# Kernel tuning notes

Hardware: AMD Instinct MI355X
Metric: run time of the kernel (lower is better)

The kernel has to match this reference:

```python
import jax, jax.numpy as jnp
import numpy as np

N = 50000      # nodes
E = 800000     # edges (before self-loops)
F_IN = 128     # num_node_features
H = 4          # heads
C = 32         # graph_hidden_channels (per head)
HC = H * C     # 128
NHID = 512
NOUT = 768
G = 256        # graphs in batch
NEG_SLOPE = 0.2


def setup_inputs() -> dict:
    key = jax.random.key(0)
    ks = jax.random.split(key, 32)
    s = 0.05
    inp = {
        "x": jax.random.normal(ks[0], (N, F_IN), jnp.float32),
        "edge_index": jax.random.randint(ks[1], (2, E), 0, N, jnp.int64),
        "batch": jnp.sort(jax.random.randint(ks[2], (N,), 0, G, jnp.int64)),
    }
    dims = [F_IN, HC, HC]
    k = 3
    for i, din in enumerate(dims, start=1):
        inp[f"w{i}"] = jax.random.normal(ks[k], (din, HC), jnp.float32) * s; k += 1
        inp[f"as{i}"] = jax.random.normal(ks[k], (H, C), jnp.float32) * s; k += 1
        inp[f"ad{i}"] = jax.random.normal(ks[k], (H, C), jnp.float32) * s; k += 1
        inp[f"b{i}"] = jnp.zeros((HC,), jnp.float32)
        inp[f"sk{i}w"] = jax.random.normal(ks[k], (din, HC), jnp.float32) * s; k += 1
        inp[f"sk{i}b"] = jnp.zeros((HC,), jnp.float32)
    inp["m1w"] = jax.random.normal(ks[k], (HC, NHID), jnp.float32) * s; k += 1
    inp["m1b"] = jnp.zeros((NHID,), jnp.float32)
    inp["m2w"] = jax.random.normal(ks[k], (NHID, NOUT), jnp.float32) * s
    inp["m2b"] = jnp.zeros((NOUT,), jnp.float32)
    return inp


def _gat_conv(x, src, dst, W, a_src, a_dst, b):
    # x: [N, din]; src/dst: [E+N] (self-loops included)
    n = x.shape[0]
    h = (x @ W).reshape(n, H, C)                       # [N, H, C]
    e_src = jnp.sum(h * a_src, axis=-1)                # [N, H]
    e_dst = jnp.sum(h * a_dst, axis=-1)                # [N, H]
    e = jax.nn.leaky_relu(e_src[src] + e_dst[dst], NEG_SLOPE)  # [E', H]
    m = jax.ops.segment_max(e, dst, num_segments=n)    # segment softmax (stable)
    ex = jnp.exp(e - m[dst])
    z = jax.ops.segment_sum(ex, dst, num_segments=n)
    alpha = ex / z[dst]                                # [E', H]
    out = jax.ops.segment_sum(alpha[:, :, None] * h[src], dst, num_segments=n)
    return out.reshape(n, HC) + b


def reference(x, edge_index, batch,
              w1, as1, ad1, b1, sk1w, sk1b,
              w2, as2, ad2, b2, sk2w, sk2b,
              w3, as3, ad3, b3, sk3w, sk3b,
              m1w, m1b, m2w, m2b):
    n = x.shape[0]
    loops = jnp.arange(n, dtype=edge_index.dtype)
    src = jnp.concatenate([edge_index[0], loops])      # PyG add_self_loops=True
    dst = jnp.concatenate([edge_index[1], loops])

    h = jax.nn.relu(x @ sk1w + sk1b + _gat_conv(x, src, dst, w1, as1, ad1, b1))
    h = jax.nn.relu(h @ sk2w + sk2b + _gat_conv(h, src, dst, w2, as2, ad2, b2))
    h = jax.nn.relu(h @ sk3w + sk3b + _gat_conv(h, src, dst, w3, as3, ad3, b3))

    pooled = jax.ops.segment_max(h, batch, num_segments=G)  # global_max_pool
    pooled = jnp.where(jnp.isfinite(pooled), pooled, 0.0)   # guard empty graphs
    out = jax.nn.relu(pooled @ m1w + m1b)
    out = out @ m2w + m2b
    return out
```

## Files before the change

### kernel.cpp

```cpp
#include <hip/hip_runtime.h>
#include <hip/hip_bf16.h>
#include <math.h>

#define NN 50000
#define EE 800000
#define EPE 850000
#define HCC 128
#define GGR 256
#define NHIDD 512
#define NOUTD 768
#define CHUNK 256
#define CPAD (CHUNK + 8)
#define SCAN_NBLK ((NN + 1023) / 1024)
#define MBLK ((NN + 63) / 64)
#define NPAD 50176
#define NREP 8

typedef __attribute__((ext_vector_type(8))) short bf16x8;
typedef __attribute__((ext_vector_type(4))) float f32x4;

__device__ __forceinline__ void atomicMaxF(float* addr, float v) {
    if (v >= 0.f) atomicMax(reinterpret_cast<int*>(addr), __float_as_int(v));
    else atomicMin(reinterpret_cast<unsigned int*>(addr), __float_as_uint(v));
}

__device__ __forceinline__ float lrelu(float x) { return x > 0.f ? x : 0.2f * x; }

__device__ __forceinline__ ushort f2bf(float f) {
    unsigned u = __float_as_uint(f);
    unsigned r = (u + 0x7fffu + ((u >> 16) & 1u)) >> 16;
    return (ushort)r;
}
__device__ __forceinline__ float bf2f(ushort b) {
    return __uint_as_float(((unsigned)b) << 16);
}

__global__ void conv_x(const float* __restrict__ X, ushort* __restrict__ Xb) {
    int i = blockIdx.x * 256 + threadIdx.x;
    if (i < NN * HCC / 4) {
        float4 v = reinterpret_cast<const float4*>(X)[i];
        ushort4 o;
        o.x = f2bf(v.x); o.y = f2bf(v.y); o.z = f2bf(v.z); o.w = f2bf(v.w);
        reinterpret_cast<ushort4*>(Xb)[i] = o;
    }
}

__global__ void conv_w(const float* __restrict__ W, const float* __restrict__ SKW,
                       ushort* __restrict__ Wt) {
    int i = blockIdx.x * 256 + threadIdx.x;
    if (i >= 256 * 128) return;
    int n = i >> 7, k = i & 127;
    float v = (n < 128) ? W[(size_t)k * 128 + n] : SKW[(size_t)k * 128 + (n - 128)];
    Wt[i] = f2bf(v);
}

__global__ void hist_zero8(int* __restrict__ cnt8) {
    int i = blockIdx.x * 256 + threadIdx.x;
    if (i < NREP * NPAD) cnt8[i] = 0;
}

__global__ void hist8(const int* __restrict__ ei, int* __restrict__ cnt8) {
    int e = blockIdx.x * 256 + threadIdx.x;
    if (e >= EPE) return;
    int rep = blockIdx.x & 7;
    int d = (e < EE) ? ei[EE + e] : e - EE;
    atomicAdd(&cnt8[rep * NPAD + d], 1);
}

__global__ __launch_bounds__(256) void scan_partial(const int* __restrict__ cnt8,
                                                    int* __restrict__ excl,
                                                    int* __restrict__ blocksums)
{
    __shared__ int s[256];
    const int b = blockIdx.x, t = threadIdx.x;
    const int idx = b * 1024 + t * 4;
    int a[4] = {0, 0, 0, 0};
    #pragma unroll
    for (int j = 0; j < 4; ++j) {
        if (idx + j < NN) {
            int tot = 0;
            #pragma unroll
            for (int r = 0; r < NREP; ++r) tot += cnt8[r * NPAD + idx + j];
            a[j] = tot;
        }
    }
    int sum4 = a[0] + a[1] + a[2] + a[3];
    s[t] = sum4;
    __syncthreads();
    #pragma unroll
    for (int off = 1; off < 256; off <<= 1) {
        int add = (t >= off) ? s[t - off] : 0;
        __syncthreads();
        s[t] += add;
        __syncthreads();
    }
    int e0 = s[t] - sum4;
    if (idx + 0 < NN) excl[idx + 0] = e0;
    if (idx + 1 < NN) excl[idx + 1] = e0 + a[0];
    if (idx + 2 < NN) excl[idx + 2] = e0 + a[0] + a[1];
    if (idx + 3 < NN) excl[idx + 3] = e0 + a[0] + a[1] + a[2];
    if (t == 255) blocksums[b] = s[255];
}

__global__ __launch_bounds__(64) void scan_sums(int* __restrict__ blocksums,
                                                int* __restrict__ blockoffs,
                                                int* __restrict__ row_start)
{
    __shared__ int s[64];
    int t = threadIdx.x;
    int v = (t < SCAN_NBLK) ? blocksums[t] : 0;
    s[t] = v;
    __syncthreads();
    #pragma unroll
    for (int off = 1; off < 64; off <<= 1) {
        int add = (t >= off) ? s[t - off] : 0;
        __syncthreads();
        s[t] += add;
        __syncthreads();
    }
    if (t < SCAN_NBLK) blockoffs[t] = s[t] - v;
    if (t == 63) row_start[NN] = s[63];
}

__global__ void scan_add(const int* __restrict__ excl, const int* __restrict__ blockoffs,
                         const int* __restrict__ cnt8,
                         int* __restrict__ row_start, int* __restrict__ cur8)
{
    int i = blockIdx.x * 256 + threadIdx.x;
    if (i >= NN) return;
    int v = excl[i] + blockoffs[i >> 10];
    row_start[i] = v;
    int c = v;
    #pragma unroll
    for (int r = 0; r < NREP; ++r) {
        cur8[r * NPAD + i] = c;
        c += cnt8[r * NPAD + i];
    }
}

__global__ void scatter_csr8(const int* __restrict__ ei, int* __restrict__ cur8,
                             int* __restrict__ csr_src) {
    int e = blockIdx.x * 256 + threadIdx.x;
    if (e >= EPE) return;
    int rep = blockIdx.x & 7;
    int s, d;
    if (e < EE) { s = ei[e]; d = ei[EE + e]; } else { s = d = e - EE; }
    int pos = atomicAdd(&cur8[rep * NPAD + d], 1);
    csr_src[pos] = s;
}

__global__ __launch_bounds__(256) void gemm_mfma(
    const ushort* __restrict__ Xb,
    const ushort* __restrict__ Wt,
    const float* __restrict__ skb, const float* __restrict__ bb,
    ushort* __restrict__ Hout, float* __restrict__ Agg)
{
    __shared__ ushort Xs[64 * 128];
    const int r0 = blockIdx.x * 64;
    const int tid = threadIdx.x;
    const int w = tid >> 6;
    const int l = tid & 63;
    const int lm = l & 15;
    const int lk = l >> 4;

    #pragma unroll
    for (int it = 0; it < 4; ++it) {
        int slot = it * 256 + tid;
        int row = slot >> 4;
        int bc = (slot & 15) << 4;
        int n = r0 + row;
        bf16x8 v = (bf16x8)(short)0;
        if (n < NN) v = *reinterpret_cast<const bf16x8*>(Xb + (size_t)n * 128 + (bc >> 1));
        *reinterpret_cast<bf16x8*>(reinterpret_cast<char*>(Xs) + row * 256 + (bc ^ ((row & 7) << 4))) = v;
    }
    __syncthreads();

    f32x4 acc[4][4];
    #pragma unroll
    for (int nb = 0; nb < 4; ++nb)
        #pragma unroll
        for (int rf = 0; rf < 4; ++rf)
            acc[nb][rf] = (f32x4){0.f, 0.f, 0.f, 0.f};

    #pragma unroll
    for (int ks = 0; ks < 4; ++ks) {
        bf16x8 a[4];
        #pragma unroll
        for (int rf = 0; rf < 4; ++rf) {
            int row = rf * 16 + lm;
            int bc = (ks * 32 + lk * 8) * 2;
            a[rf] = *reinterpret_cast<const bf16x8*>(
                reinterpret_cast<const char*>(Xs) + row * 256 + (bc ^ ((row & 7) << 4)));
        }
        #pragma unroll
        for (int nb = 0; nb < 4; ++nb) {
            int ncol = (w * 4 + nb) * 16 + lm;
            bf16x8 b = *reinterpret_cast<const bf16x8*>(Wt + (size_t)ncol * 128 + ks * 32 + lk * 8);
            #pragma unroll
            for (int rf = 0; rf < 4; ++rf)
                acc[nb][rf] = __builtin_amdgcn_mfma_f32_16x16x32_bf16(a[rf], b, acc[nb][rf], 0, 0, 0);
        }
    }

    #pragma unroll
    for (int nb = 0; nb < 4; ++nb) {
        int ncol = (w * 4 + nb) * 16 + lm;
        #pragma unroll
        for (int rf = 0; rf < 4; ++rf) {
            #pragma unroll
            for (int r = 0; r < 4; ++r) {
                int n = r0 + rf * 16 + lk * 4 + r;
                if (n >= NN) continue;
                float v = acc[nb][rf][r];
                if (ncol < 128) {
                    Hout[(size_t)n * 128 + ncol] = f2bf(v);
                } else {
                    int c = ncol - 128;
                    Agg[(size_t)n * 128 + c] = v + skb[c] + bb[c];
                }
            }
        }
    }
}

__global__ __launch_bounds__(256) void node_attn(
    const ushort* __restrict__ Hb, const float* __restrict__ as_, const float* __restrict__ ad_,
    float* __restrict__ esrc, float* __restrict__ edst)
{
    int tid = threadIdx.x;
    int node = blockIdx.x * 2 + (tid >> 7);
    int t = tid & 127;
    if (node >= NN) return;
    float hv = bf2f(Hb[(size_t)node * 128 + t]);
    float p1 = hv * as_[t];
    float p2 = hv * ad_[t];
    #pragma unroll
    for (int o = 16; o > 0; o >>= 1) {
        p1 += __shfl_down(p1, o, 32);
        p2 += __shfl_down(p2, o, 32);
    }
    if ((t & 31) == 0) {
        esrc[node * 4 + (t >> 5)] = p1;
        edst[node * 4 + (t >> 5)] = p2;
    }
}

__global__ __launch_bounds__(128) void gat_aggr(
    const int* __restrict__ row_start, const int* __restrict__ csr_src,
    const float* __restrict__ esrc, const float* __restrict__ edst,
    const ushort* __restrict__ Hb, const float* __restrict__ skipagg,
    ushort* __restrict__ outbuf)
{
    __shared__ int   lsrc[CHUNK];
    __shared__ float lw[4][CPAD];
    __shared__ float shsc[4];
    __shared__ float accbuf[8][HCC];
    const int d = blockIdx.x;
    const int t = threadIdx.x;
    const int hd = t >> 5;
    const int l = t & 31;
    const int slot = t >> 4;
    const int cg = t & 15;
    const int c0 = cg * 8;
    const int ghd = cg >> 2;
    const int r0 = row_start[d], r1 = row_start[d + 1];
    const float4 edv = *reinterpret_cast<const float4*>(edst + (size_t)d * 4);
    float acc[8] = {0.f, 0.f, 0.f, 0.f, 0.f, 0.f, 0.f, 0.f};
    float m_h = -INFINITY, z_h = 0.f;

    for (int base = r0; base < r1; base += CHUNK) {
        const int nc = min(CHUNK, r1 - base);
        __syncthreads();
        for (int i = t; i < nc; i += 128) {
            int s = csr_src[base + i];
            lsrc[i] = s;
            float4 ev = *reinterpret_cast<const float4*>(esrc + (size_t)s * 4);
            lw[0][i] = lrelu(ev.x + edv.x);
            lw[1][i] = lrelu(ev.y + edv.y);
            lw[2][i] = lrelu(ev.z + edv.z);
            lw[3][i] = lrelu(ev.w + edv.w);
        }
        __syncthreads();
        float mx = m_h;
        for (int i = l; i < nc; i += 32) mx = fmaxf(mx, lw[hd][i]);
        #pragma unroll
        for (int off = 16; off > 0; off >>= 1) mx = fmaxf(mx, __shfl_xor(mx, off, 32));
        float sc = __expf(m_h - mx);
        float zp = 0.f;
        for (int i = l; i < nc; i += 32) {
            float w = __expf(lw[hd][i] - mx);
            lw[hd][i] = w;
            zp += w;
        }
        #pragma unroll
        for (int off = 16; off > 0; off >>= 1) zp += __shfl_xor(zp, off, 32);
        z_h = z_h * sc + zp;
        m_h = mx;
        if (l == 0) shsc[hd] = sc;
        __syncthreads();
        float scg = shsc[ghd];
        #pragma unroll
        for (int j = 0; j < 8; ++j) acc[j] *= scg;
        for (int i = slot; i < nc; i += 8) {
            int s = lsrc[i];
            float wgt = lw[ghd][i];
            bf16x8 row = *reinterpret_cast<const bf16x8*>(Hb + (size_t)s * 128 + c0);
            #pragma unroll
            for (int j = 0; j < 8; ++j)
                acc[j] = fmaf(wgt, bf2f((ushort)row[j]), acc[j]);
        }
    }
    #pragma unroll
    for (int j = 0; j < 8; ++j) accbuf[slot][c0 + j] = acc[j];
    __syncthreads();
    float tot = 0.f;
    #pragma unroll
    for (int s = 0; s < 8; ++s) tot += accbuf[s][t];
    float res = skipagg[(size_t)d * 128 + t] + tot / z_h;
    outbuf[(size_t)d * 128 + t] = f2bf(fmaxf(res, 0.f));
}

__global__ void pool_init(float* __restrict__ pooled) {
    int i = blockIdx.x * 256 + threadIdx.x;
    if (i < GGR * HCC) pooled[i] = -INFINITY;
}

__global__ __launch_bounds__(256) void pool_max_sorted(
    const ushort* __restrict__ xf, const int* __restrict__ batch,
    float* __restrict__ pooled)
{
    __shared__ int gb[32];
    const int n0 = blockIdx.x * 32;
    const int t = threadIdx.x;
    if (t < 32) gb[t] = (n0 + t < NN) ? batch[n0 + t] : -1;
    __syncthreads();
    const int c = t & 127;
    const int half = t >> 7;
    int curg = -1;
    float curv = -INFINITY;
    #pragma unroll 4
    for (int i = 0; i < 16; ++i) {
        int n = n0 + half * 16 + i;
        if (n >= NN) break;
        int g = gb[half * 16 + i];
        float v = bf2f(xf[(size_t)n * 128 + c]);
        if (g != curg) {
            if (curg >= 0) atomicMaxF(&pooled[curg * 128 + c], curv);
            curg = g; curv = v;
        } else {
            curv = fmaxf(curv, v);
        }
    }
    if (curg >= 0) atomicMaxF(&pooled[curg * 128 + c], curv);
}

__global__ __launch_bounds__(512) void mlp1(const float* __restrict__ pooled,
                                            const float* __restrict__ w,
                                            const float* __restrict__ bias,
                                            float* __restrict__ hid)
{
    __shared__ float xs[128];
    int g = blockIdx.x, t = threadIdx.x;
    if (t < 128) {
        float v = pooled[g * 128 + t];
        if (!isfinite(v)) v = 0.f;
        xs[t] = v;
    }
    __syncthreads();
    float acc = 0.f;
    #pragma unroll 8
    for (int k = 0; k < 128; ++k) acc += xs[k] * w[(size_t)k * NHIDD + t];
    hid[(size_t)g * NHIDD + t] = fmaxf(acc + bias[t], 0.f);
}

__global__ __launch_bounds__(768) void mlp2(const float* __restrict__ hid,
                                            const float* __restrict__ w,
                                            const float* __restrict__ bias,
                                            float* __restrict__ out)
{
    __shared__ float xs[NHIDD];
    int g = blockIdx.x, t = threadIdx.x;
    if (t < NHIDD) xs[t] = hid[(size_t)g * NHIDD + t];
    __syncthreads();
    float acc = 0.f;
    #pragma unroll 8
    for (int k = 0; k < NHIDD; ++k) acc += xs[k] * w[(size_t)k * NOUTD + t];
    out[(size_t)g * NOUTD + t] = acc + bias[t];
}

extern "C" void kernel_launch(void* const* d_in, const int* in_sizes, int n_in,
                              void* d_out, int out_size, void* d_ws, size_t ws_size,
                              hipStream_t stream)
{
    const float* x = (const float*)d_in[0];
    const int* ei = (const int*)d_in[1];
    const int* batch = (const int*)d_in[2];
    const float* W[3]   = {(const float*)d_in[3],  (const float*)d_in[9],  (const float*)d_in[15]};
    const float* AS[3]  = {(const float*)d_in[4],  (const float*)d_in[10], (const float*)d_in[16]};
    const float* AD[3]  = {(const float*)d_in[5],  (const float*)d_in[11], (const float*)d_in[17]};
    const float* B[3]   = {(const float*)d_in[6],  (const float*)d_in[12], (const float*)d_in[18]};
    const float* SKW[3] = {(const float*)d_in[7],  (const float*)d_in[13], (const float*)d_in[19]};
    const float* SKB[3] = {(const float*)d_in[8],  (const float*)d_in[14], (const float*)d_in[20]};
    const float* m1w = (const float*)d_in[21];
    const float* m1b = (const float*)d_in[22];
    const float* m2w = (const float*)d_in[23];
    const float* m2b = (const float*)d_in[24];
    float* out = (float*)d_out;

    float* p = (float*)d_ws;
    ushort* bufA = (ushort*)p; p += (size_t)NN * HCC / 2;
    ushort* bufB = (ushort*)p; p += (size_t)NN * HCC / 2;
    ushort* xb   = (ushort*)p; p += (size_t)NN * HCC / 2;
    ushort* hbuf = (ushort*)p; p += (size_t)NN * HCC / 2;
    ushort* wt3  = (ushort*)p; p += 3 * 256 * 128 / 2;
    float* agg  = p; p += (size_t)NN * HCC;
    float* esrc = p; p += NN * 4;
    float* edst = p; p += NN * 4;
    float* pooled = p; p += GGR * HCC;
    float* hidden = p; p += GGR * NHIDD;
    int* cnt8      = (int*)p; p += NREP * NPAD;
    int* cur8      = (int*)p; p += NREP * NPAD;
    int* excl      = (int*)p; p += NN;
    int* row_start = (int*)p; p += NN + 4;
    int* csr_src   = (int*)p; p += EPE;
    int* blocksums = (int*)p; p += 64;
    int* blockoffs = (int*)p; p += 64;

    conv_x<<<(NN * HCC / 4 + 255) / 256, 256, 0, stream>>>(x, xb);
    for (int l = 0; l < 3; ++l)
        conv_w<<<(256 * 128 + 255) / 256, 256, 0, stream>>>(W[l], SKW[l], wt3 + l * 256 * 128);

    hist_zero8<<<(NREP * NPAD + 255) / 256, 256, 0, stream>>>(cnt8);
    hist8<<<(EPE + 255) / 256, 256, 0, stream>>>(ei, cnt8);
    scan_partial<<<SCAN_NBLK, 256, 0, stream>>>(cnt8, excl, blocksums);
    scan_sums<<<1, 64, 0, stream>>>(blocksums, blockoffs, row_start);
    scan_add<<<(NN + 255) / 256, 256, 0, stream>>>(excl, blockoffs, cnt8, row_start, cur8);
    scatter_csr8<<<(EPE + 255) / 256, 256, 0, stream>>>(ei, cur8, csr_src);

    const ushort* cur = xb;
    ushort* outs[3] = {bufA, bufB, bufA};
    for (int l = 0; l < 3; ++l) {
        gemm_mfma<<<MBLK, 256, 0, stream>>>(cur, wt3 + l * 256 * 128, SKB[l], B[l], hbuf, agg);
        node_attn<<<NN / 2, 256, 0, stream>>>(hbuf, AS[l], AD[l], esrc, edst);
        gat_aggr<<<NN, 128, 0, stream>>>(row_start, csr_src, esrc, edst, hbuf, agg, outs[l]);
        cur = outs[l];
    }
    pool_init<<<(GGR * HCC) / 256, 256, 0, stream>>>(pooled);
    pool_max_sorted<<<(NN + 31) / 32, 256, 0, stream>>>(cur, batch, pooled);
    mlp1<<<GGR, NHIDD, 0, stream>>>(pooled, m1w, m1b, hidden);
    mlp2<<<GGR, NOUTD, 0, stream>>>(hidden, m2w, m2b, out);
}
```

Before: 528.0 us.

## Fuse attention logits into GEMM epilogue and partition CSR scatter by destination

Computes per-node source/destination attention logits directly from the GEMM accumulators via wave shuffles, removing the separate node_attn kernel and its reread of the hidden features each layer. Replaces the replicated-cursor CSR scatter with a scatter where each block handles one of eight destination ranges, improving atomic locality at the cost of reading the destination array eight times. Logits now come from fp32 accumulators instead of rounded bf16 values.

Result: faster. 494.1 us (-6.4%).

```diff
diff --git a/kernel.cpp b/kernel.cpp
--- a/kernel.cpp
+++ b/kernel.cpp
@@ -15,6 +15,7 @@
 #define MBLK ((NN + 63) / 64)
 #define NPAD 50176
 #define NREP 8
+#define NPART (NN / 8)
 
 typedef __attribute__((ext_vector_type(8))) short bf16x8;
 typedef __attribute__((ext_vector_type(4))) float f32x4;
@@ -123,39 +124,49 @@
 }
 
 __global__ void scan_add(const int* __restrict__ excl, const int* __restrict__ blockoffs,
-                         const int* __restrict__ cnt8,
-                         int* __restrict__ row_start, int* __restrict__ cur8)
+                         int* __restrict__ row_start, int* __restrict__ cursor)
 {
     int i = blockIdx.x * 256 + threadIdx.x;
     if (i >= NN) return;
     int v = excl[i] + blockoffs[i >> 10];
     row_start[i] = v;
-    int c = v;
-    #pragma unroll
-    for (int r = 0; r < NREP; ++r) {
-        cur8[r * NPAD + i] = c;
-        c += cnt8[r * NPAD + i];
-    }
-}
-
-__global__ void scatter_csr8(const int* __restrict__ ei, int* __restrict__ cur8,
-                             int* __restrict__ csr_src) {
-    int e = blockIdx.x * 256 + threadIdx.x;
-    if (e >= EPE) return;
-    int rep = blockIdx.x & 7;
-    int s, d;
-    if (e < EE) { s = ei[e]; d = ei[EE + e]; } else { s = d = e - EE; }
-    int pos = atomicAdd(&cur8[rep * NPAD + d], 1);
-    csr_src[pos] = s;
+    cursor[i] = v;
+}
+
+__global__ __launch_bounds__(256) void scatter_part(const int* __restrict__ ei,
+                                                    int* __restrict__ cursor,
+                                                    int* __restrict__ csr_src)
+{
+    const int p = blockIdx.x & 7;
+    const int q = blockIdx.x >> 3;
+    const int nq = gridDim.x >> 3;
+    const int lo = p * NPART, hi = lo + NPART;
+    const int stride = nq * 256;
+    for (int e = q * 256 + threadIdx.x; e < EE; e += stride) {
+        int d = ei[EE + e];
+        if (d >= lo && d < hi) {
+            int s = ei[e];
+            int pos = atomicAdd(&cursor[d], 1);
+            csr_src[pos] = s;
+        }
+    }
+    for (int i = q * 256 + threadIdx.x; i < NPART; i += stride) {
+        int d = lo + i;
+        int pos = atomicAdd(&cursor[d], 1);
+        csr_src[pos] = d;
+    }
 }
 
 __global__ __launch_bounds__(256) void gemm_mfma(
     const ushort* __restrict__ Xb,
     const ushort* __restrict__ Wt,
     const float* __restrict__ skb, const float* __restrict__ bb,
-    ushort* __restrict__ Hout, float* __restrict__ Agg)
+    const float* __restrict__ as_, const float* __restrict__ ad_,
+    ushort* __restrict__ Hout, float* __restrict__ Agg,
+    float* __restrict__ esrc, float* __restrict__ edst)
 {
     __shared__ ushort Xs[64 * 128];
+    __shared__ float sh_es[64][4], sh_ed[64][4];
     const int r0 = blockIdx.x * 64;
     const int tid = threadIdx.x;
     const int w = tid >> 6;
@@ -202,46 +213,64 @@
         }
     }
 
-    #pragma unroll
-    for (int nb = 0; nb < 4; ++nb) {
-        int ncol = (w * 4 + nb) * 16 + lm;
+    if (w < 2) {
+        float asv[4], adv[4];
+        #pragma unroll
+        for (int nb = 0; nb < 4; ++nb) {
+            int ncol = (w * 4 + nb) * 16 + lm;
+            asv[nb] = as_[ncol];
+            adv[nb] = ad_[ncol];
+        }
         #pragma unroll
         for (int rf = 0; rf < 4; ++rf) {
             #pragma unroll
             for (int r = 0; r < 4; ++r) {
-                int n = r0 + rf * 16 + lk * 4 + r;
-                if (n >= NN) continue;
-                float v = acc[nb][rf][r];
-                if (ncol < 128) {
-                    Hout[(size_t)n * 128 + ncol] = f2bf(v);
-                } else {
-                    int c = ncol - 128;
-                    Agg[(size_t)n * 128 + c] = v + skb[c] + bb[c];
+                int nl = rf * 16 + lk * 4 + r;
+                int n = r0 + nl;
+                float es0 = 0.f, es1 = 0.f, ed0 = 0.f, ed1 = 0.f;
+                #pragma unroll
+                for (int nb = 0; nb < 4; ++nb) {
+                    float v = acc[nb][rf][r];
+                    int ncol = (w * 4 + nb) * 16 + lm;
+                    if (n < NN) Hout[(size_t)n * 128 + ncol] = f2bf(v);
+                    if (nb < 2) { es0 = fmaf(v, asv[nb], es0); ed0 = fmaf(v, adv[nb], ed0); }
+                    else        { es1 = fmaf(v, asv[nb], es1); ed1 = fmaf(v, adv[nb], ed1); }
+                }
+                #pragma unroll
+                for (int m = 1; m < 16; m <<= 1) {
+                    es0 += __shfl_xor(es0, m); ed0 += __shfl_xor(ed0, m);
+                    es1 += __shfl_xor(es1, m); ed1 += __shfl_xor(ed1, m);
+                }
+                if (lm == 0) {
+                    sh_es[nl][w * 2 + 0] = es0; sh_ed[nl][w * 2 + 0] = ed0;
+                    sh_es[nl][w * 2 + 1] = es1; sh_ed[nl][w * 2 + 1] = ed1;
                 }
             }
         }
-    }
-}
-
-__global__ __launch_bounds__(256) void node_attn(
-    const ushort* __restrict__ Hb, const float* __restrict__ as_, const float* __restrict__ ad_,
-    float* __restrict__ esrc, float* __restrict__ edst)
-{
-    int tid = threadIdx.x;
-    int node = blockIdx.x * 2 + (tid >> 7);
-    int t = tid & 127;
-    if (node >= NN) return;
-    float hv = bf2f(Hb[(size_t)node * 128 + t]);
-    float p1 = hv * as_[t];
-    float p2 = hv * ad_[t];
-    #pragma unroll
-    for (int o = 16; o > 0; o >>= 1) {
-        p1 += __shfl_down(p1, o, 32);
-        p2 += __shfl_down(p2, o, 32);
-    }
-    if ((t & 31) == 0) {
-        esrc[node * 4 + (t >> 5)] = p1;
-        edst[node * 4 + (t >> 5)] = p2;
+    } else {
+        #pragma unroll
+        for (int nb = 0; nb < 4; ++nb) {
+            int ncol = (w * 4 + nb) * 16 + lm;
+            int c = ncol - 128;
+            #pragma unroll
+            for (int rf = 0; rf < 4; ++rf) {
+                #pragma unroll
+                for (int r = 0; r < 4; ++r) {
+                    int n = r0 + rf * 16 + lk * 4 + r;
+                    if (n >= NN) continue;
+                    Agg[(size_t)n * 128 + c] = acc[nb][rf][r] + skb[c] + bb[c];
+                }
+            }
+        }
+    }
+    __syncthreads();
+    if (tid < 256) {
+        int nl = tid >> 2, hd = tid & 3;
+        int n = r0 + nl;
+        if (n < NN) {
+            esrc[n * 4 + hd] = sh_es[nl][hd];
+            edst[n * 4 + hd] = sh_ed[nl][hd];
+        }
     }
 }
 
@@ -419,7 +448,7 @@
     float* pooled = p; p += GGR * HCC;
     float* hidden = p; p += GGR * NHIDD;
     int* cnt8      = (int*)p; p += NREP * NPAD;
-    int* cur8      = (int*)p; p += NREP * NPAD;
+    int* cursor    = (int*)p; p += NN;
     int* excl      = (int*)p; p += NN;
     int* row_start = (int*)p; p += NN + 4;
     int* csr_src   = (int*)p; p += EPE;
@@ -434,14 +463,14 @@
     hist8<<<(EPE + 255) / 256, 256, 0, stream>>>(ei, cnt8);
     scan_partial<<<SCAN_NBLK, 256, 0, stream>>>(cnt8, excl, blocksums);
     scan_sums<<<1, 64, 0, stream>>>(blocksums, blockoffs, row_start);
-    scan_add<<<(NN + 255) / 256, 256, 0, stream>>>(excl, blockoffs, cnt8, row_start, cur8);
-    scatter_csr8<<<(EPE + 255) / 256, 256, 0, stream>>>(ei, cur8, csr_src);
+    scan_add<<<(NN + 255) / 256, 256, 0, stream>>>(excl, blockoffs, row_start, cursor);
+    scatter_part<<<1024, 256, 0, stream>>>(ei, cursor, csr_src);
 
     const ushort* cur = xb;
     ushort* outs[3] = {bufA, bufB, bufA};
     for (int l = 0; l < 3; ++l) {
-        gemm_mfma<<<MBLK, 256, 0, stream>>>(cur, wt3 + l * 256 * 128, SKB[l], B[l], hbuf, agg);
-        node_attn<<<NN / 2, 256, 0, stream>>>(hbuf, AS[l], AD[l], esrc, edst);
+        gemm_mfma<<<MBLK, 256, 0, stream>>>(cur, wt3 + l * 256 * 128, SKB[l], B[l],
+                                            AS[l], AD[l], hbuf, agg, esrc, edst);
         gat_aggr<<<NN, 128, 0, stream>>>(row_start, csr_src, esrc, edst, hbuf, agg, outs[l]);
         cur = outs[l];
     }
```
